# Kernel tuning notes

Hardware: AMD Instinct MI355X
Metric: run time of the kernel (lower is better)

The kernel has to match this reference:

```python
import jax, jax.numpy as jnp
import numpy as np

HEADS = 8
SR = 2
EPS_BN = 1e-5
EPS_LN = 1e-5


def _conv(x, w, b, stride=1, pad=0):
    y = jax.lax.conv_general_dilated(x, w, (stride, stride), [(pad, pad), (pad, pad)],
                                     dimension_numbers=('NCHW', 'OIHW', 'NCHW'))
    return y + b[None, :, None, None]


def _bn(x, g, b):
    # eval-mode BatchNorm with running_mean=0, running_var=1
    return x * (g / jnp.sqrt(1.0 + EPS_BN))[None, :, None, None] + b[None, :, None, None]


def _dwt_haar(x):
    # [B,c,H,W] -> [B,4c,H/2,W/2] stacked as LL,HL,LH,HH (Wave-ViT convention)
    x1 = x[:, :, 0::2, 0::2] / 2
    x2 = x[:, :, 1::2, 0::2] / 2
    x3 = x[:, :, 0::2, 1::2] / 2
    x4 = x[:, :, 1::2, 1::2] / 2
    ll = x1 + x2 + x3 + x4
    hl = -x1 - x2 + x3 + x4
    lh = -x1 + x2 - x3 + x4
    hh = x1 - x2 - x3 + x4
    return jnp.concatenate([ll, hl, lh, hh], axis=1)


def _idwt_haar(y):
    # [B,4c,h,w] -> [B,c,2h,2w], exact inverse of _dwt_haar
    c = y.shape[1] // 4
    ll, hl, lh, hh = y[:, :c], y[:, c:2 * c], y[:, 2 * c:3 * c], y[:, 3 * c:]
    p1 = (ll - hl - lh + hh) / 2  # (0::2, 0::2)
    p2 = (ll - hl + lh - hh) / 2  # (1::2, 0::2)
    p3 = (ll + hl - lh - hh) / 2  # (0::2, 1::2)
    p4 = (ll + hl + lh + hh) / 2  # (1::2, 1::2)
    B, _, h2, w2 = ll.shape
    row0 = jnp.stack([p1, p3], axis=-1)  # even rows
    row1 = jnp.stack([p2, p4], axis=-1)  # odd rows
    out = jnp.stack([row0, row1], axis=3)  # [B,c,h2,2,w2,2]
    return out.reshape(B, c, 2 * h2, 2 * w2)


def setup_inputs() -> dict:
    key = jax.random.key(0)
    ks = jax.random.split(key, 12)
    B, H, W, C = 8, 56, 56, 512
    N = H * W
    c4 = C // 4

    def nrm(k, shp, std):
        return jax.random.normal(k, shp, jnp.float32) * std

    return {
        'x': jax.random.normal(ks[0], (B, N, C), jnp.float32),
        'H': H, 'W': W,
        'reduce_w': nrm(ks[1], (c4, C, 1, 1), (2.0 / c4) ** 0.5),
        'reduce_b': jnp.zeros((c4,), jnp.float32),
        'reduce_g': jnp.ones((c4,), jnp.float32),
        'reduce_beta': jnp.zeros((c4,), jnp.float32),
        'filter_w': nrm(ks[2], (C, C, 3, 3), (2.0 / (9 * C)) ** 0.5),
        'filter_b': jnp.zeros((C,), jnp.float32),
        'filter_g': jnp.ones((C,), jnp.float32),
        'filter_beta': jnp.zeros((C,), jnp.float32),
        'q_w': nrm(ks[3], (C, C), 0.02),
        'q_b': jnp.zeros((C,), jnp.float32),
        'ln_g': jnp.ones((C,), jnp.float32),
        'ln_b': jnp.zeros((C,), jnp.float32),
        'kv_w': nrm(ks[4], (2 * C, C), 0.02),
        'kv_b': jnp.zeros((2 * C,), jnp.float32),
        'kve_w': nrm(ks[5], (C, C, SR, SR), (2.0 / (SR * SR * C)) ** 0.5),
        'kve_b': jnp.zeros((C,), jnp.float32),
        'proj_w': nrm(ks[6], (C, C + c4), 0.02),
        'proj_b': jnp.zeros((C,), jnp.float32),
    }


def reference(x, H, W, reduce_w, reduce_b, reduce_g, reduce_beta,
              filter_w, filter_b, filter_g, filter_beta,
              q_w, q_b, ln_g, ln_b, kv_w, kv_b, kve_w, kve_b, proj_w, proj_b):
    B, N, C = x.shape
    hd = C // HEADS
    scale = hd ** -0.5

    q = (x @ q_w.T + q_b).reshape(B, N, HEADS, hd).transpose(0, 2, 1, 3)  # [B,h,N,d]

    xi = x.reshape(B, H, W, C).transpose(0, 3, 1, 2)  # NCHW
    r = jax.nn.relu(_bn(_conv(xi, reduce_w, reduce_b), reduce_g, reduce_beta))  # [B,C/4,H,W]
    r16 = r.astype(jnp.float16)
    x_dwt = _dwt_haar(r16).astype(jnp.float32)  # [B,C,H/2,W/2]
    x_dwt = jax.nn.relu(_bn(_conv(x_dwt, filter_w, filter_b, pad=1), filter_g, filter_beta))
    x_dwt16 = x_dwt.astype(jnp.float16)
    x_idwt = _idwt_haar(x_dwt16)  # [B,C/4,H,W] fp16
    x_idwt = x_idwt.reshape(B, C // 4, H * W).transpose(0, 2, 1)  # [B,N,C/4]

    x_dwt = x_dwt16.astype(jnp.float32)
    kv_in = _conv(x_dwt, kve_w, kve_b, stride=SR).reshape(B, C, -1).transpose(0, 2, 1)  # [B,M,C]
    mu = kv_in.mean(-1, keepdims=True)
    var = ((kv_in - mu) ** 2).mean(-1, keepdims=True)
    kv_n = (kv_in - mu) / jnp.sqrt(var + EPS_LN) * ln_g + ln_b
    kv = (kv_n @ kv_w.T + kv_b).reshape(B, -1, 2, HEADS, hd).transpose(2, 0, 3, 1, 4)
    k, v = kv[0], kv[1]  # [B,h,M,d]

    attn = jax.nn.softmax(jnp.einsum('bhnd,bhmd->bhnm', q, k) * scale, axis=-1)
    o = jnp.einsum('bhnm,bhmd->bhnd', attn, v).transpose(0, 2, 1, 3).reshape(B, N, C)
    o = jnp.concatenate([o, x_idwt.astype(jnp.float32)], axis=-1)  # [B,N,C+C/4]
    return o @ proj_w.T + proj_b
```

## Files before the change

### kernel.cpp

```cpp
#include <hip/hip_runtime.h>
#include <math.h>


typedef _Float16 half8 __attribute__((ext_vector_type(8)));
typedef float f32x4 __attribute__((ext_vector_type(4)));

static const size_t OFF_X16  = 0;
static const size_t OFF_Q16  = 12845056;
static const size_t OFF_CAT  = 25690112;
static const size_t OFF_R16  = 41746432;
static const size_t OFF_PAD  = 44957696;
static const size_t OFF_DWTB = 48644096;
static const size_t OFF_QRW  = 51855360;
static const size_t OFF_LN16 = 55066624;
static const size_t OFF_KV16 = 55869440;
static const size_t OFF_WT   = 57475072;
static const size_t OFF_KT   = 59834368;
static const size_t OFF_KVW  = 61145088;
static const size_t OFF_PW   = 61669376;
static const size_t OFF_VT   = 62062592;
static const size_t OFF_PART = 62980096;

#define BN_RSQ 0.9999950000374997f
#define SCL2   0.1803368801111204f
#define PART_STRIDE 3211264
#define KVE_STRIDE  802816

__device__ __forceinline__ void async_copy16(const _Float16* g, _Float16* l) {
    __builtin_amdgcn_global_load_lds(
        (const __attribute__((address_space(1))) void*)g,
        (__attribute__((address_space(3))) void*)l, 16, 0, 0);
}

#define WAIT4_BARRIER() asm volatile("s_waitcnt vmcnt(4)\n\ts_barrier" ::: "memory")
#define WAIT6_BARRIER() asm volatile("s_waitcnt vmcnt(6)\n\ts_barrier" ::: "memory")
#define WAIT0_BARRIER() asm volatile("s_waitcnt vmcnt(0)\n\ts_barrier" ::: "memory")

template <int ALOAD, int EPI>
__global__ __launch_bounds__(256) void gemm16(
    const _Float16* __restrict__ A, const _Float16* __restrict__ W,
    void* __restrict__ outp, int M, int K, int lda, int ldc,
    const float* __restrict__ bias, void* __restrict__ outp2)
{
    __shared__ _Float16 sA[3][128 * 32];
    __shared__ _Float16 sB[3][128 * 32];
    const int t = threadIdx.x;
    const int lane = t & 63, wid = t >> 6;

    int bx = blockIdx.x, by = blockIdx.y;
    const int m0 = bx * 128, n0 = by * 128;
    const int kbase = blockIdx.z * K;

    const int sr = wid * 16 + (lane >> 2);
    const int sc = (lane & 3) * 8;
    const int stA0 = wid * 512;
    const int stA1 = 2048 + wid * 512;

    const _Float16 *aP0, *aP1;
    if constexpr (ALOAD == 0) {
        int r0 = m0 + sr;      if (r0 > M - 1) r0 = M - 1;
        int r1 = m0 + 64 + sr; if (r1 > M - 1) r1 = M - 1;
        aP0 = A + (size_t)r0 * lda + sc;
        aP1 = A + (size_t)r1 * lda + sc;
    } else {
        int m_ = m0 + sr; if (m_ > M - 1) m_ = M - 1;
        int b_ = m_ / 196, rem = m_ - b_ * 196, i_ = rem / 14, j_ = rem - i_ * 14;
        aP0 = A + ((size_t)(b_ * 784 + 2 * i_ * 28 + 2 * j_)) * 512 + sc;
        m_ = m0 + 64 + sr; if (m_ > M - 1) m_ = M - 1;
        b_ = m_ / 196; rem = m_ - b_ * 196; i_ = rem / 14; j_ = rem - i_ * 14;
        aP1 = A + ((size_t)(b_ * 784 + 2 * i_ * 28 + 2 * j_)) * 512 + sc;
    }
    const int ldw = (ALOAD == 2) ? lda : K;
    const _Float16* bP0 = W + (size_t)(n0 + sr) * ldw + sc;
    const _Float16* bP1 = W + (size_t)(n0 + 64 + sr) * ldw + sc;

    const int mw = wid & 1, nw = wid >> 1;
    const int pAoff = (mw * 64 + (lane & 15)) * 32 + (lane >> 4) * 8;
    const int pBoff = (nw * 64 + (lane & 15)) * 32 + (lane >> 4) * 8;

    f32x4 acc[4][4];
#pragma unroll
    for (int i = 0; i < 4; ++i)
#pragma unroll
        for (int j = 0; j < 4; ++j) acc[i][j] = (f32x4)(0.0f);

    auto aoff_of = [&](int k) -> int {
        if constexpr (ALOAD == 0) {
            return k;
        } else {
            int sub = k >> 9; int ky = sub >> 1, kx = sub & 1;
            return (ky * 28 + kx) * 512 + (k & 511);
        }
    };
    auto stage = [&](int ti, int buf) {
        int k = kbase + ti * 32;
        int aOff = aoff_of(k);
        async_copy16(aP0 + aOff, &sA[buf][stA0]);
        async_copy16(aP1 + aOff, &sA[buf][stA1]);
        async_copy16(bP0 + k, &sB[buf][stA0]);
        async_copy16(bP1 + k, &sB[buf][stA1]);
    };

    const int nt = K >> 5;
    stage(0, 0);
    if (nt > 1) { stage(1, 1); WAIT4_BARRIER(); }
    else        { WAIT0_BARRIER(); }

    int cur = 0;
    for (int i = 0; i < nt; ++i) {
        const _Float16* pA = &sA[cur][0] + pAoff;
        const _Float16* pB = &sB[cur][0] + pBoff;
        half8 aF[4], bF[4];
#pragma unroll
        for (int u = 0; u < 4; ++u) aF[u] = *(const half8*)(pA + u * 512);
#pragma unroll
        for (int u = 0; u < 4; ++u) bF[u] = *(const half8*)(pB + u * 512);

        const bool st = (i + 2 < nt);
        if (st) {
            int nb = cur + 2; if (nb >= 3) nb -= 3;
            stage(i + 2, nb);
        }
#pragma unroll
        for (int u = 0; u < 4; ++u)
#pragma unroll
            for (int j = 0; j < 4; ++j)
                acc[u][j] = __builtin_amdgcn_mfma_f32_16x16x32_f16(
                    aF[u], bF[j], acc[u][j], 0, 0, 0);

        if (i + 1 < nt) {
            if (st) WAIT4_BARRIER();
            else    WAIT0_BARRIER();
        }
        ++cur; if (cur == 3) cur = 0;
    }

    const int orow = m0 + mw * 64 + (lane >> 4) * 4;
    const int ocol = n0 + nw * 64 + (lane & 15);
#pragma unroll
    for (int j = 0; j < 4; ++j) {
        int col = ocol + j * 16;
        float bv = 0.0f;
        if constexpr (EPI == 5) bv = bias[col];
#pragma unroll
        for (int i = 0; i < 4; ++i) {
#pragma unroll
            for (int r = 0; r < 4; ++r) {
                int row = orow + i * 16 + r;
                if (row >= M) continue;
                float v = acc[i][j][r] + bv;
                if constexpr (EPI == 3) {
                    ((float*)outp)[(size_t)blockIdx.z * KVE_STRIDE
                                   + (size_t)row * ldc + col] = v;
                } else {
                    if (n0 >= 512) {
                        int hd_ = col - 512;
                        int h_ = hd_ >> 6, d_ = hd_ & 63;
                        int b_ = row / 196, m_ = row - b_ * 196;
                        ((_Float16*)outp2)[((size_t)((b_ * 8 + h_) * 64 + d_)) * 224
                                           + m_] = (_Float16)v;
                    } else {
                        ((_Float16*)outp)[(size_t)row * ldc + col] = (_Float16)v;
                    }
                }
            }
        }
    }
}

template <int EPI>
__global__ __launch_bounds__(256) void gemm16f(
    const _Float16* __restrict__ A, const _Float16* __restrict__ W,
    void* __restrict__ outp, int M, int K, int lda, int ldc,
    const float* __restrict__ bias, const float* __restrict__ bng,
    const float* __restrict__ bnb, const float* __restrict__ bias2,
    void* __restrict__ outp2)
{
    __shared__ _Float16 sA[3][256 * 32];
    __shared__ _Float16 sB[3][128 * 32];
    const int t = threadIdx.x;
    const int lane = t & 63, wid = t >> 6;

    int bx = blockIdx.x, by = blockIdx.y;
    {
        int nwg = gridDim.x * gridDim.y;
        if ((nwg & 7) == 0) {
            int orig = by * gridDim.x + bx;
            int cs = nwg >> 3;
            int wg = (orig & 7) * cs + (orig >> 3);
            by = wg % gridDim.y;
            bx = wg / gridDim.y;
        }
    }
    const int m0 = bx * 256, n0 = by * 128;

    const int sr = wid * 16 + (lane >> 2);
    const int sc = (lane & 3) * 8;
    const int stO = wid * 512;

    const _Float16* aP[4];
#pragma unroll
    for (int g = 0; g < 4; ++g) {
        int r_ = m0 + g * 64 + sr; if (r_ > M - 1) r_ = M - 1;
        aP[g] = A + (size_t)r_ * lda + sc;
    }
    const _Float16* bP0 = W + (size_t)(n0 + sr) * K + sc;
    const _Float16* bP1 = W + (size_t)(n0 + 64 + sr) * K + sc;

    const int mw = wid & 1, nw = wid >> 1;
    const int pAoff = (mw * 128 + (lane & 15)) * 32 + (lane >> 4) * 8;
    const int pBoff = (nw * 64 + (lane & 15)) * 32 + (lane >> 4) * 8;

    f32x4 acc[8][4];
#pragma unroll
    for (int i = 0; i < 8; ++i)
#pragma unroll
        for (int j = 0; j < 4; ++j) acc[i][j] = (f32x4)(0.0f);

    auto stage = [&](int ti, int buf) {
        int k = ti * 32;
#pragma unroll
        for (int g = 0; g < 4; ++g)
            async_copy16(aP[g] + k, &sA[buf][g * 2048 + stO]);
        async_copy16(bP0 + k, &sB[buf][stO]);
        async_copy16(bP1 + k, &sB[buf][2048 + stO]);
    };

    const int nt = K >> 5;
    stage(0, 0);
    stage(1, 1);
    WAIT6_BARRIER();

    int cur = 0;
    for (int i = 0; i < nt; ++i) {
        const _Float16* pA = &sA[cur][0] + pAoff;
        const _Float16* pB = &sB[cur][0] + pBoff;
        half8 aF[8], bF[4];
#pragma unroll
        for (int u = 0; u < 8; ++u) aF[u] = *(const half8*)(pA + u * 512);
#pragma unroll
        for (int u = 0; u < 4; ++u) bF[u] = *(const half8*)(pB + u * 512);

        const bool st = (i + 2 < nt);
        if (st) {
            int nb = cur + 2; if (nb >= 3) nb -= 3;
            stage(i + 2, nb);
        }
#pragma unroll
        for (int u = 0; u < 8; ++u)
#pragma unroll
            for (int j = 0; j < 4; ++j)
                acc[u][j] = __builtin_amdgcn_mfma_f32_16x16x32_f16(
                    aF[u], bF[j], acc[u][j], 0, 0, 0);

        if (i + 1 < nt) {
            if (st) WAIT6_BARRIER();
            else    WAIT0_BARRIER();
        }
        ++cur; if (cur == 3) cur = 0;
    }

    const int orow = m0 + mw * 128 + (lane >> 4) * 4;
    const int ocol = n0 + nw * 64 + (lane & 15);
#pragma unroll
    for (int j = 0; j < 4; ++j) {
        int col = ocol + j * 16;
        float bv = 0.0f, g = 0.0f, b2 = 0.0f;
        if constexpr (EPI == 4) {
            if (n0 >= 512) {
                bv = bias2[col - 512];
                g = bng[col - 512] * BN_RSQ;
                b2 = bnb[col - 512];
            } else {
                bv = bias[col];
            }
        } else {
            bv = bias[col];
        }
#pragma unroll
        for (int i = 0; i < 8; ++i) {
#pragma unroll
            for (int r = 0; r < 4; ++r) {
                int row = orow + i * 16 + r;
                if (row >= M) continue;
                float v = acc[i][j][r] + bv;
                if constexpr (EPI == 0) {
                    __builtin_nontemporal_store(
                        v, (float*)outp + (size_t)row * ldc + col);
                } else {
                    if (n0 >= 512) {
                        v = fmaxf(v * g + b2, 0.0f);
                        ((_Float16*)outp2)[(size_t)row * 128 + (col - 512)] =
                            (_Float16)v;
                    } else {
                        ((_Float16*)outp)[(size_t)row * ldc + col] = (_Float16)v;
                    }
                }
            }
        }
    }
}

__global__ __launch_bounds__(256) void conv_splitk_fat(
    const _Float16* __restrict__ A, const _Float16* __restrict__ W,
    float* __restrict__ partA, float* __restrict__ partB)
{
    __shared__ _Float16 sA[3][256 * 32];
    __shared__ _Float16 sB[3][128 * 32];
    const int t = threadIdx.x;
    const int lane = t & 63, wid = t >> 6;

    int orig = blockIdx.x;
    int wg = (orig & 7) * 50 + (orig >> 3);
    int bx = wg % 25;  int c = wg / 25;
    int by = c & 3,    bz = c >> 2;

    const int m0 = bx * 256, n0 = by * 128;
    const int kbase = bz * 1152;

    const int sr = wid * 16 + (lane >> 2);
    const int sc = (lane & 3) * 8;
    const int stO = wid * 512;

    const _Float16* aP[4];
#pragma unroll
    for (int g = 0; g < 4; ++g) {
        int m_ = m0 + g * 64 + sr; if (m_ > 6271) m_ = 6271;
        int b_ = m_ / 784, rem = m_ - b_ * 784, y_ = rem / 28, x_ = rem - y_ * 28;
        aP[g] = A + ((size_t)(b_ * 900 + (y_ + 1) * 30 + (x_ + 1))) * 512 + sc;
    }
    const _Float16* bP0 = W + (size_t)(n0 + sr) * 4608 + sc;
    const _Float16* bP1 = W + (size_t)(n0 + 64 + sr) * 4608 + sc;

    const int mw = wid & 1, nw = wid >> 1;
    const int pAoff = (mw * 128 + (lane & 15)) * 32 + (lane >> 4) * 8;
    const int pBoff = (nw * 64 + (lane & 15)) * 32 + (lane >> 4) * 8;

    f32x4 acc[8][4];
#pragma unroll
    for (int i = 0; i < 8; ++i)
#pragma unroll
        for (int j = 0; j < 4; ++j) acc[i][j] = (f32x4)(0.0f);

    auto aoff_of = [&](int k) -> int {
        int sub = k >> 9; int s3 = sub / 3;
        int dy = s3 - 1, dx = sub - s3 * 3 - 1;
        return (dy * 30 + dx) * 512 + (k & 511);
    };
    auto stage = [&](int ti, int buf) {
        int k = kbase + ti * 32;
        int aOff = aoff_of(k);
#pragma unroll
        for (int g = 0; g < 4; ++g)
            async_copy16(aP[g] + aOff, &sA[buf][g * 2048 + stO]);
        async_copy16(bP0 + k, &sB[buf][stO]);
        async_copy16(bP1 + k, &sB[buf][2048 + stO]);
    };

    const int nt = 36;
    stage(0, 0);
    stage(1, 1);
    WAIT6_BARRIER();

    int cur = 0;
    for (int i = 0; i < nt; ++i) {
        const _Float16* pA = &sA[cur][0] + pAoff;
        const _Float16* pB = &sB[cur][0] + pBoff;
        half8 aF[8], bF[4];
#pragma unroll
        for (int u = 0; u < 8; ++u) aF[u] = *(const half8*)(pA + u * 512);
#pragma unroll
        for (int u = 0; u < 4; ++u) bF[u] = *(const half8*)(pB + u * 512);

        const bool st = (i + 2 < nt);
        if (st) {
            int nb = cur + 2; if (nb >= 3) nb -= 3;
            stage(i + 2, nb);
        }
#pragma unroll
        for (int u = 0; u < 8; ++u)
#pragma unroll
            for (int j = 0; j < 4; ++j)
                acc[u][j] = __builtin_amdgcn_mfma_f32_16x16x32_f16(
                    aF[u], bF[j], acc[u][j], 0, 0, 0);

        if (i + 1 < nt) {
            if (st) WAIT6_BARRIER();
            else    WAIT0_BARRIER();
        }
        ++cur; if (cur == 3) cur = 0;
    }

    float* dst = (bz < 2) ? (partA + (size_t)bz * PART_STRIDE)
                          : (partB + (size_t)(bz - 2) * PART_STRIDE);
    const int orow = m0 + mw * 128 + (lane >> 4) * 4;
    const int ocol = n0 + nw * 64 + (lane & 15);
#pragma unroll
    for (int j = 0; j < 4; ++j) {
#pragma unroll
        for (int i = 0; i < 8; ++i) {
#pragma unroll
            for (int r = 0; r < 4; ++r) {
                int row = orow + i * 16 + r;
                if (row < 6272)
                    dst[(size_t)row * 512 + ocol + j * 16] = acc[i][j][r];
            }
        }
    }
}

__global__ __launch_bounds__(128) void conv_epi_idwt(
    const float* __restrict__ pA, const float* __restrict__ pB,
    _Float16* __restrict__ dwtb, _Float16* __restrict__ cat,
    const float* __restrict__ bias, const float* __restrict__ bng,
    const float* __restrict__ bnb)
{
    int p = blockIdx.x;
    int b = p / 784; int rem = p - b * 784;
    int i = rem / 28;  int j = rem - i * 28;
    int c = threadIdx.x;
    size_t base = (size_t)p * 512;
    _Float16 g16[4];
#pragma unroll
    for (int g = 0; g < 4; ++g) {
        int ch = g * 128 + c;
        float s = (pA[base + ch] + pA[PART_STRIDE + base + ch])
                + (pB[base + ch] + pB[PART_STRIDE + base + ch]);
        float v = (s + bias[ch]) * (bng[ch] * BN_RSQ) + bnb[ch];
        g16[g] = (_Float16)fmaxf(v, 0.0f);
        dwtb[base + ch] = g16[g];
    }
    _Float16 ll = g16[0], hl = g16[1], lh = g16[2], hh = g16[3];
    _Float16 h = (_Float16)0.5f;
    _Float16 p1 = (((ll - hl) - lh) + hh) * h;
    _Float16 p2 = (((ll - hl) + lh) - hh) * h;
    _Float16 p3 = (((ll + hl) - lh) - hh) * h;
    _Float16 p4 = (((ll + hl) + lh) + hh) * h;
    int y = 2 * i, x = 2 * j;
    size_t rb = (size_t)b * 3136;
    __builtin_nontemporal_store(p1, &cat[(rb + (size_t)y * 56 + x) * 640 + 512 + c]);
    __builtin_nontemporal_store(p3, &cat[(rb + (size_t)y * 56 + x + 1) * 640 + 512 + c]);
    __builtin_nontemporal_store(p2, &cat[(rb + (size_t)(y + 1) * 56 + x) * 640 + 512 + c]);
    __builtin_nontemporal_store(p4, &cat[(rb + (size_t)(y + 1) * 56 + x + 1) * 640 + 512 + c]);
}

__device__ __forceinline__ void cvt8_at(
    const float* __restrict__ s, _Float16* __restrict__ d, int i)
{
    const float4* sp = (const float4*)(s + (size_t)i * 8);
    float4 a = sp[0], b = sp[1];
    half8 h;
    h[0] = (_Float16)a.x; h[1] = (_Float16)a.y; h[2] = (_Float16)a.z; h[3] = (_Float16)a.w;
    h[4] = (_Float16)b.x; h[5] = (_Float16)b.y; h[6] = (_Float16)b.z; h[7] = (_Float16)b.w;
    *(half8*)(d + (size_t)i * 8) = h;
}

__global__ __launch_bounds__(256) void prep_kernel(
    const float* __restrict__ qw, const float* __restrict__ rw,
    const float* __restrict__ kvw, const float* __restrict__ pw,
    const float* __restrict__ fw, const float* __restrict__ kw,
    const float* __restrict__ x,
    _Float16* __restrict__ qrw16, _Float16* __restrict__ kvw16,
    _Float16* __restrict__ pw16, _Float16* __restrict__ wT,
    _Float16* __restrict__ kT, _Float16* __restrict__ pad,
    _Float16* __restrict__ vt, _Float16* __restrict__ x16)
{
    int bid = blockIdx.x, tid = threadIdx.x;
    if (bid < 128) {
        cvt8_at(qw, qrw16, bid * 256 + tid);
    } else if (bid < 160) {
        cvt8_at(rw, qrw16 + 262144, (bid - 128) * 256 + tid);
    } else if (bid < 416) {
        cvt8_at(kvw, kvw16, (bid - 160) * 256 + tid);
    } else if (bid < 576) {
        cvt8_at(pw, pw16, (bid - 416) * 256 + tid);
    } else if (bid < 9792) {
        int idx = (bid - 576) * 256 + tid;
        int n = idx / 4608; int r = idx - n * 4608;
        int sub = r >> 9; int ci = r & 511;
        wT[idx] = (_Float16)fw[(size_t)n * 4608 + ci * 9 + sub];
    } else if (bid < 13888) {
        int idx = (bid - 9792) * 256 + tid;
        int n = idx >> 11; int r = idx & 2047;
        int sub = r >> 9; int ci = r & 511;
        kT[idx] = (_Float16)kw[((size_t)n << 11) + (ci << 2) + sub];
    } else if (bid < 15688) {
        int i = (bid - 13888) * 256 + tid;
        *(float4*)(pad + (size_t)i * 8) = make_float4(0.f, 0.f, 0.f, 0.f);
    } else if (bid < 16136) {
        int i = (bid - 15688) * 256 + tid;
        *(float4*)(vt + (size_t)i * 8) = make_float4(0.f, 0.f, 0.f, 0.f);
    } else {
        cvt8_at(x, x16, (bid - 16136) * 256 + tid);
    }
}

__global__ __launch_bounds__(128) void dwt_kernel(
    const _Float16* __restrict__ r, _Float16* __restrict__ pad)
{
    int bid = blockIdx.x;
    int b = bid / 784; int rem = bid - b * 784;
    int i = rem / 28;  int j = rem - i * 28;
    int c = threadIdx.x;
    int y = 2 * i, x = 2 * j;
    size_t base = (size_t)b * 3136;
    _Float16 f1 = r[(base + (size_t)y * 56 + x) * 128 + c];
    _Float16 f2 = r[(base + (size_t)(y + 1) * 56 + x) * 128 + c];
    _Float16 f3 = r[(base + (size_t)y * 56 + (x + 1)) * 128 + c];
    _Float16 f4 = r[(base + (size_t)(y + 1) * 56 + (x + 1)) * 128 + c];
    _Float16 h = (_Float16)0.5f;
    _Float16 x1 = f1 * h, x2 = f2 * h, x3 = f3 * h, x4 = f4 * h;
    _Float16 ll = ((x1 + x2) + x3) + x4;
    _Float16 hl = (((-x1) - x2) + x3) + x4;
    _Float16 lh = (((-x1) + x2) - x3) + x4;
    _Float16 hh = ((x1 - x2) - x3) + x4;
    size_t ob = ((size_t)b * 900 + (size_t)(i + 1) * 30 + (j + 1)) * 512;
    pad[ob + c]       = ll;
    pad[ob + 128 + c] = hl;
    pad[ob + 256 + c] = lh;
    pad[ob + 384 + c] = hh;
}

__global__ __launch_bounds__(256) void ln_kernel(
    const float* __restrict__ part, _Float16* __restrict__ o,
    const float* __restrict__ g, const float* __restrict__ bta,
    const float* __restrict__ kvb)
{
    int wave = threadIdx.x >> 6;
    int lane = threadIdx.x & 63;
    int row = blockIdx.x * 4 + wave;
    int c = lane * 8;
    const float* rp = part + (size_t)row * 512 + c;
    float v[8];
#pragma unroll
    for (int i = 0; i < 8; i += 4) {
        float4 a0 = *(const float4*)(rp + i);
        float4 a1 = *(const float4*)(rp + KVE_STRIDE + i);
        float4 a2 = *(const float4*)(rp + 2 * KVE_STRIDE + i);
        float4 a3 = *(const float4*)(rp + 3 * KVE_STRIDE + i);
        v[i + 0] = (a0.x + a1.x) + (a2.x + a3.x) + kvb[c + i + 0];
        v[i + 1] = (a0.y + a1.y) + (a2.y + a3.y) + kvb[c + i + 1];
        v[i + 2] = (a0.z + a1.z) + (a2.z + a3.z) + kvb[c + i + 2];
        v[i + 3] = (a0.w + a1.w) + (a2.w + a3.w) + kvb[c + i + 3];
    }
    float s = ((v[0] + v[1]) + (v[2] + v[3])) + ((v[4] + v[5]) + (v[6] + v[7]));
#pragma unroll
    for (int off = 32; off; off >>= 1) s += __shfl_xor(s, off);
    float mu = s * (1.0f / 512.0f);
    float sq = 0.0f;
#pragma unroll
    for (int i = 0; i < 8; ++i) { v[i] -= mu; sq += v[i] * v[i]; }
#pragma unroll
    for (int off = 32; off; off >>= 1) sq += __shfl_xor(sq, off);
    float inv = 1.0f / sqrtf(sq * (1.0f / 512.0f) + 1e-5f);
    half8 hv;
#pragma unroll
    for (int i = 0; i < 8; ++i) hv[i] = (_Float16)(v[i] * inv * g[c + i] + bta[c + i]);
    *(half8*)(o + (size_t)row * 512 + c) = hv;
}

__global__ __launch_bounds__(256) void attn_mfma(
    const _Float16* __restrict__ q, const _Float16* __restrict__ kv,
    const _Float16* __restrict__ vt, _Float16* __restrict__ cat)
{
    __shared__ _Float16 sK[64][72];
    __shared__ _Float16 sVT[64][72];
    __shared__ _Float16 sP[4][16][40];
    int bid = blockIdx.x;
    int qt = bid % 49;
    int h  = (bid / 49) & 7;
    int b  = bid / 392;
    int n0 = qt * 64;
    int t = threadIdx.x, lane = t & 63, wid = t >> 6;
    int quad = lane >> 4, l16 = lane & 15;

    const _Float16* qp = q + ((size_t)(b * 3136 + n0 + wid * 16 + l16)) * 512
                           + h * 64 + quad * 8;
    half8 aQ0 = *(const half8*)qp;
    half8 aQ1 = *(const half8*)(qp + 32);

    f32x4 oacc[4];
#pragma unroll
    for (int i = 0; i < 4; ++i) oacc[i] = (f32x4)(0.0f);
    float lsum[4] = {0.f, 0.f, 0.f, 0.f};

    const _Float16* vtb = vt + ((size_t)((b * 8 + h) * 64)) * 224;

    for (int c0 = 0; c0 < 224; c0 += 64) {
        __syncthreads();
#pragma unroll
        for (int it = 0; it < 2; ++it) {
            int slot = t + 256 * it;
            int row = slot >> 3, c8 = (slot & 7) * 8;
            int m = c0 + row; if (m > 195) m = 195;
            *(half8*)&sK[row][c8] =
                *(const half8*)(kv + ((size_t)(b * 196 + m)) * 1024 + h * 64 + c8);
        }
#pragma unroll
        for (int it = 0; it < 2; ++it) {
            int slot = t + 256 * it;
            int row = slot >> 3, c8 = (slot & 7) * 8;
            *(half8*)&sVT[row][c8] =
                *(const half8*)(vtb + (size_t)row * 224 + c0 + c8);
        }
        __syncthreads();

#pragma unroll
        for (int sc = 0; sc < 64; sc += 32) {
            half8 bk00 = *(const half8*)&sK[sc + l16][quad * 8];
            half8 bk01 = *(const half8*)&sK[sc + l16][32 + quad * 8];
            half8 bk10 = *(const half8*)&sK[sc + 16 + l16][quad * 8];
            half8 bk11 = *(const half8*)&sK[sc + 16 + l16][32 + quad * 8];
            f32x4 s0 = (f32x4)(0.0f), s1 = (f32x4)(0.0f);
            s0 = __builtin_amdgcn_mfma_f32_16x16x32_f16(aQ0, bk00, s0, 0, 0, 0);
            s0 = __builtin_amdgcn_mfma_f32_16x16x32_f16(aQ1, bk01, s0, 0, 0, 0);
            s1 = __builtin_amdgcn_mfma_f32_16x16x32_f16(aQ0, bk10, s1, 0, 0, 0);
            s1 = __builtin_amdgcn_mfma_f32_16x16x32_f16(aQ1, bk11, s1, 0, 0, 0);

            int col0 = c0 + sc + l16;
            float msk0 = (col0 < 196) ? 0.0f : -INFINITY;
            float msk1 = (col0 + 16 < 196) ? 0.0f : -INFINITY;
            float p0[4], p1[4];
#pragma unroll
            for (int r = 0; r < 4; ++r) {
                p0[r] = exp2f(s0[r] * SCL2 + msk0);
                p1[r] = exp2f(s1[r] * SCL2 + msk1);
                lsum[r] += p0[r] + p1[r];
            }
#pragma unroll
            for (int r = 0; r < 4; ++r) {
                sP[wid][quad * 4 + r][l16]      = (_Float16)p0[r];
                sP[wid][quad * 4 + r][16 + l16] = (_Float16)p1[r];
            }
            half8 aP = *(const half8*)&sP[wid][l16][quad * 8];
            half8 bv0 = *(const half8*)&sVT[l16][sc + quad * 8];
            half8 bv1 = *(const half8*)&sVT[16 + l16][sc + quad * 8];
            half8 bv2 = *(const half8*)&sVT[32 + l16][sc + quad * 8];
            half8 bv3 = *(const half8*)&sVT[48 + l16][sc + quad * 8];
            oacc[0] = __builtin_amdgcn_mfma_f32_16x16x32_f16(aP, bv0, oacc[0], 0, 0, 0);
            oacc[1] = __builtin_amdgcn_mfma_f32_16x16x32_f16(aP, bv1, oacc[1], 0, 0, 0);
            oacc[2] = __builtin_amdgcn_mfma_f32_16x16x32_f16(aP, bv2, oacc[2], 0, 0, 0);
            oacc[3] = __builtin_amdgcn_mfma_f32_16x16x32_f16(aP, bv3, oacc[3], 0, 0, 0);
        }
    }

    float inv[4];
#pragma unroll
    for (int r = 0; r < 4; ++r) {
        float s = lsum[r];
        s += __shfl_xor(s, 1);
        s += __shfl_xor(s, 2);
        s += __shfl_xor(s, 4);
        s += __shfl_xor(s, 8);
        inv[r] = 1.0f / s;
    }
#pragma unroll
    for (int r = 0; r < 4; ++r) {
        size_t rowoff = ((size_t)(b * 3136 + n0 + wid * 16 + quad * 4 + r)) * 640
                        + h * 64 + l16;
#pragma unroll
        for (int tv = 0; tv < 4; ++tv)
            cat[rowoff + tv * 16] = (_Float16)(oacc[tv][r] * inv[r]);
    }
}

extern "C" void kernel_launch(void* const* d_in, const int* in_sizes, int n_in,
                              void* d_out, int out_size, void* d_ws, size_t ws_size,
                              hipStream_t stream)
{
    const float* x           = (const float*)d_in[0];
    const float* reduce_w    = (const float*)d_in[3];
    const float* reduce_b    = (const float*)d_in[4];
    const float* reduce_g    = (const float*)d_in[5];
    const float* reduce_beta = (const float*)d_in[6];
    const float* filter_w    = (const float*)d_in[7];
    const float* filter_b    = (const float*)d_in[8];
    const float* filter_g    = (const float*)d_in[9];
    const float* filter_beta = (const float*)d_in[10];
    const float* q_w         = (const float*)d_in[11];
    const float* q_b         = (const float*)d_in[12];
    const float* ln_g        = (const float*)d_in[13];
    const float* ln_b        = (const float*)d_in[14];
    const float* kv_w        = (const float*)d_in[15];
    const float* kv_b        = (const float*)d_in[16];
    const float* kve_w       = (const float*)d_in[17];
    const float* kve_b       = (const float*)d_in[18];
    const float* proj_w      = (const float*)d_in[19];
    const float* proj_b      = (const float*)d_in[20];
    float* out = (float*)d_out;
    _Float16* hws = (_Float16*)d_ws;

    _Float16* x16    = hws + OFF_X16;
    _Float16* q16    = hws + OFF_Q16;
    _Float16* cat16  = hws + OFF_CAT;
    _Float16* r16    = hws + OFF_R16;
    _Float16* pad16  = hws + OFF_PAD;
    _Float16* dwtb16 = hws + OFF_DWTB;
    _Float16* qrw16  = hws + OFF_QRW;
    _Float16* ln16   = hws + OFF_LN16;
    _Float16* kv16   = hws + OFF_KV16;
    _Float16* wT16   = hws + OFF_WT;
    _Float16* kT16   = hws + OFF_KT;
    _Float16* kvw16  = hws + OFF_KVW;
    _Float16* pw16   = hws + OFF_PW;
    _Float16* vt16   = hws + OFF_VT;
    float*    partA  = (float*)(hws + OFF_X16);
    float*    partB  = (float*)(hws + OFF_PART);
    float*    kvepart = (float*)(hws + OFF_X16);

    prep_kernel<<<dim3(22408), dim3(256), 0, stream>>>(
        q_w, reduce_w, kv_w, proj_w, filter_w, kve_w, x,
        qrw16, kvw16, pw16, wT16, kT16, pad16, vt16, x16);

    gemm16f<4><<<dim3(98, 5), dim3(256), 0, stream>>>(
        x16, qrw16, q16, 25088, 512, 512, 512, q_b, reduce_g, reduce_beta,
        reduce_b, r16);

    dwt_kernel<<<dim3(6272), dim3(128), 0, stream>>>(r16, pad16);

    conv_splitk_fat<<<dim3(400), dim3(256), 0, stream>>>(pad16, wT16, partA, partB);

    conv_epi_idwt<<<dim3(6272), dim3(128), 0, stream>>>(
        partA, partB, dwtb16, cat16, filter_b, filter_g, filter_beta);

    gemm16<2, 3><<<dim3(13, 4, 4), dim3(256), 0, stream>>>(
        dwtb16, kT16, kvepart, 1568, 512, 2048, 512, nullptr, nullptr);

    ln_kernel<<<dim3(392), dim3(256), 0, stream>>>(kvepart, ln16, ln_g, ln_b, kve_b);

    gemm16<0, 5><<<dim3(13, 8), dim3(256), 0, stream>>>(
        ln16, kvw16, kv16, 1568, 512, 512, 1024, kv_b, vt16);

    attn_mfma<<<dim3(3136), dim3(256), 0, stream>>>(q16, kv16, vt16, cat16);

    gemm16f<0><<<dim3(98, 4), dim3(256), 0, stream>>>(
        cat16, pw16, out, 25088, 640, 640, 512, proj_b, nullptr, nullptr,
        nullptr, nullptr);
}
```

Before: 443.2 us.

## Shrink GEMM and conv tiles to 128x128 with eight waves, add MFMA priority hints

The fat 256x128 GEMM and split-K conv kernels become 128x128 tiles run by 512 threads (eight waves), each wave computing a 64x32 sub-tile with fewer accumulators. Grids double to raise occupancy and spread work across more CUs, at the cost of less data reuse per tile and more LDS traffic per FLOP. Attention MFMA blocks are also wrapped in s_setprio to favour the matrix instructions during scheduling. The conv kernel drops its row clamp and bounds check, which relies on 6272 rows dividing evenly into 128-row tiles.

```diff
diff --git a/kernel.cpp b/kernel.cpp
--- a/kernel.cpp
+++ b/kernel.cpp
@@ -33,7 +33,7 @@
 }
 
 #define WAIT4_BARRIER() asm volatile("s_waitcnt vmcnt(4)\n\ts_barrier" ::: "memory")
-#define WAIT6_BARRIER() asm volatile("s_waitcnt vmcnt(6)\n\ts_barrier" ::: "memory")
+#define WAIT2_BARRIER() asm volatile("s_waitcnt vmcnt(2)\n\ts_barrier" ::: "memory")
 #define WAIT0_BARRIER() asm volatile("s_waitcnt vmcnt(0)\n\ts_barrier" ::: "memory")
 
 template <int ALOAD, int EPI>
@@ -169,14 +169,14 @@
 }
 
 template <int EPI>
-__global__ __launch_bounds__(256) void gemm16f(
+__global__ __launch_bounds__(512) void gemm16w8(
     const _Float16* __restrict__ A, const _Float16* __restrict__ W,
     void* __restrict__ outp, int M, int K, int lda, int ldc,
     const float* __restrict__ bias, const float* __restrict__ bng,
     const float* __restrict__ bnb, const float* __restrict__ bias2,
     void* __restrict__ outp2)
 {
-    __shared__ _Float16 sA[3][256 * 32];
+    __shared__ _Float16 sA[3][128 * 32];
     __shared__ _Float16 sB[3][128 * 32];
     const int t = threadIdx.x;
     const int lane = t & 63, wid = t >> 6;
@@ -192,54 +192,46 @@
             bx = wg / gridDim.y;
         }
     }
-    const int m0 = bx * 256, n0 = by * 128;
+    const int m0 = bx * 128, n0 = by * 128;
 
     const int sr = wid * 16 + (lane >> 2);
     const int sc = (lane & 3) * 8;
     const int stO = wid * 512;
 
-    const _Float16* aP[4];
-#pragma unroll
-    for (int g = 0; g < 4; ++g) {
-        int r_ = m0 + g * 64 + sr; if (r_ > M - 1) r_ = M - 1;
-        aP[g] = A + (size_t)r_ * lda + sc;
-    }
-    const _Float16* bP0 = W + (size_t)(n0 + sr) * K + sc;
-    const _Float16* bP1 = W + (size_t)(n0 + 64 + sr) * K + sc;
+    int r0 = m0 + sr; if (r0 > M - 1) r0 = M - 1;
+    const _Float16* aP = A + (size_t)r0 * lda + sc;
+    const _Float16* bP = W + (size_t)(n0 + sr) * K + sc;
 
     const int mw = wid & 1, nw = wid >> 1;
-    const int pAoff = (mw * 128 + (lane & 15)) * 32 + (lane >> 4) * 8;
-    const int pBoff = (nw * 64 + (lane & 15)) * 32 + (lane >> 4) * 8;
-
-    f32x4 acc[8][4];
-#pragma unroll
-    for (int i = 0; i < 8; ++i)
-#pragma unroll
-        for (int j = 0; j < 4; ++j) acc[i][j] = (f32x4)(0.0f);
+    const int pAoff = (mw * 64 + (lane & 15)) * 32 + (lane >> 4) * 8;
+    const int pBoff = (nw * 32 + (lane & 15)) * 32 + (lane >> 4) * 8;
+
+    f32x4 acc[4][2];
+#pragma unroll
+    for (int i = 0; i < 4; ++i)
+#pragma unroll
+        for (int j = 0; j < 2; ++j) acc[i][j] = (f32x4)(0.0f);
 
     auto stage = [&](int ti, int buf) {
         int k = ti * 32;
-#pragma unroll
-        for (int g = 0; g < 4; ++g)
-            async_copy16(aP[g] + k, &sA[buf][g * 2048 + stO]);
-        async_copy16(bP0 + k, &sB[buf][stO]);
-        async_copy16(bP1 + k, &sB[buf][2048 + stO]);
+        async_copy16(aP + k, &sA[buf][stO]);
+        async_copy16(bP + k, &sB[buf][stO]);
     };
 
     const int nt = K >> 5;
     stage(0, 0);
     stage(1, 1);
-    WAIT6_BARRIER();
+    WAIT2_BARRIER();
 
     int cur = 0;
     for (int i = 0; i < nt; ++i) {
         const _Float16* pA = &sA[cur][0] + pAoff;
         const _Float16* pB = &sB[cur][0] + pBoff;
-        half8 aF[8], bF[4];
-#pragma unroll
-        for (int u = 0; u < 8; ++u) aF[u] = *(const half8*)(pA + u * 512);
-#pragma unroll
-        for (int u = 0; u < 4; ++u) bF[u] = *(const half8*)(pB + u * 512);
+        half8 aF[4], bF[2];
+#pragma unroll
+        for (int u = 0; u < 4; ++u) aF[u] = *(const half8*)(pA + u * 512);
+#pragma unroll
+        for (int v = 0; v < 2; ++v) bF[v] = *(const half8*)(pB + v * 512);
 
         const bool st = (i + 2 < nt);
         if (st) {
@@ -247,25 +239,25 @@
             stage(i + 2, nb);
         }
 #pragma unroll
-        for (int u = 0; u < 8; ++u)
-#pragma unroll
-            for (int j = 0; j < 4; ++j)
-                acc[u][j] = __builtin_amdgcn_mfma_f32_16x16x32_f16(
-                    aF[u], bF[j], acc[u][j], 0, 0, 0);
+        for (int u = 0; u < 4; ++u)
+#pragma unroll
+            for (int v = 0; v < 2; ++v)
+                acc[u][v] = __builtin_amdgcn_mfma_f32_16x16x32_f16(
+                    aF[u], bF[v], acc[u][v], 0, 0, 0);
 
         if (i + 1 < nt) {
-            if (st) WAIT6_BARRIER();
+            if (st) WAIT2_BARRIER();
             else    WAIT0_BARRIER();
         }
         ++cur; if (cur == 3) cur = 0;
     }
 
-    const int orow = m0 + mw * 128 + (lane >> 4) * 4;
-    const int ocol = n0 + nw * 64 + (lane & 15);
-#pragma unroll
-    for (int j = 0; j < 4; ++j) {
-        int col = ocol + j * 16;
-        float bv = 0.0f, g = 0.0f, b2 = 0.0f;
+    const int orow = m0 + mw * 64 + (lane >> 4) * 4;
+    const int ocol = n0 + nw * 32 + (lane & 15);
+#pragma unroll
+    for (int v = 0; v < 2; ++v) {
+        int col = ocol + v * 16;
+        float bv, g = 0.0f, b2 = 0.0f;
         if constexpr (EPI == 4) {
             if (n0 >= 512) {
                 bv = bias2[col - 512];
@@ -278,22 +270,22 @@
             bv = bias[col];
         }
 #pragma unroll
-        for (int i = 0; i < 8; ++i) {
+        for (int u = 0; u < 4; ++u) {
 #pragma unroll
             for (int r = 0; r < 4; ++r) {
-                int row = orow + i * 16 + r;
+                int row = orow + u * 16 + r;
                 if (row >= M) continue;
-                float v = acc[i][j][r] + bv;
+                float v2 = acc[u][v][r] + bv;
                 if constexpr (EPI == 0) {
                     __builtin_nontemporal_store(
-                        v, (float*)outp + (size_t)row * ldc + col);
+                        v2, (float*)outp + (size_t)row * ldc + col);
                 } else {
                     if (n0 >= 512) {
-                        v = fmaxf(v * g + b2, 0.0f);
+                        v2 = fmaxf(v2 * g + b2, 0.0f);
                         ((_Float16*)outp2)[(size_t)row * 128 + (col - 512)] =
-                            (_Float16)v;
+                            (_Float16)v2;
                     } else {
-                        ((_Float16*)outp)[(size_t)row * ldc + col] = (_Float16)v;
+                        ((_Float16*)outp)[(size_t)row * ldc + col] = (_Float16)v2;
                     }
                 }
             }
@@ -301,46 +293,41 @@
     }
 }
 
-__global__ __launch_bounds__(256) void conv_splitk_fat(
+__global__ __launch_bounds__(512) void conv_splitk(
     const _Float16* __restrict__ A, const _Float16* __restrict__ W,
     float* __restrict__ partA, float* __restrict__ partB)
 {
-    __shared__ _Float16 sA[3][256 * 32];
+    __shared__ _Float16 sA[3][128 * 32];
     __shared__ _Float16 sB[3][128 * 32];
     const int t = threadIdx.x;
     const int lane = t & 63, wid = t >> 6;
 
     int orig = blockIdx.x;
-    int wg = (orig & 7) * 50 + (orig >> 3);
-    int bx = wg % 25;  int c = wg / 25;
+    int wg = (orig & 7) * 98 + (orig >> 3);
+    int bx = wg % 49;  int c = wg / 49;
     int by = c & 3,    bz = c >> 2;
 
-    const int m0 = bx * 256, n0 = by * 128;
+    const int m0 = bx * 128, n0 = by * 128;
     const int kbase = bz * 1152;
 
     const int sr = wid * 16 + (lane >> 2);
     const int sc = (lane & 3) * 8;
     const int stO = wid * 512;
 
-    const _Float16* aP[4];
-#pragma unroll
-    for (int g = 0; g < 4; ++g) {
-        int m_ = m0 + g * 64 + sr; if (m_ > 6271) m_ = 6271;
-        int b_ = m_ / 784, rem = m_ - b_ * 784, y_ = rem / 28, x_ = rem - y_ * 28;
-        aP[g] = A + ((size_t)(b_ * 900 + (y_ + 1) * 30 + (x_ + 1))) * 512 + sc;
-    }
-    const _Float16* bP0 = W + (size_t)(n0 + sr) * 4608 + sc;
-    const _Float16* bP1 = W + (size_t)(n0 + 64 + sr) * 4608 + sc;
+    int m_ = m0 + sr;
+    int b_ = m_ / 784, rem = m_ - b_ * 784, y_ = rem / 28, x_ = rem - y_ * 28;
+    const _Float16* aP = A + ((size_t)(b_ * 900 + (y_ + 1) * 30 + (x_ + 1))) * 512 + sc;
+    const _Float16* bP = W + (size_t)(n0 + sr) * 4608 + sc;
 
     const int mw = wid & 1, nw = wid >> 1;
-    const int pAoff = (mw * 128 + (lane & 15)) * 32 + (lane >> 4) * 8;
-    const int pBoff = (nw * 64 + (lane & 15)) * 32 + (lane >> 4) * 8;
-
-    f32x4 acc[8][4];
-#pragma unroll
-    for (int i = 0; i < 8; ++i)
-#pragma unroll
-        for (int j = 0; j < 4; ++j) acc[i][j] = (f32x4)(0.0f);
+    const int pAoff = (mw * 64 + (lane & 15)) * 32 + (lane >> 4) * 8;
+    const int pBoff = (nw * 32 + (lane & 15)) * 32 + (lane >> 4) * 8;
+
+    f32x4 acc[4][2];
+#pragma unroll
+    for (int i = 0; i < 4; ++i)
+#pragma unroll
+        for (int j = 0; j < 2; ++j) acc[i][j] = (f32x4)(0.0f);
 
     auto aoff_of = [&](int k) -> int {
         int sub = k >> 9; int s3 = sub / 3;
@@ -349,28 +336,24 @@
     };
     auto stage = [&](int ti, int buf) {
         int k = kbase + ti * 32;
-        int aOff = aoff_of(k);
-#pragma unroll
-        for (int g = 0; g < 4; ++g)
-            async_copy16(aP[g] + aOff, &sA[buf][g * 2048 + stO]);
-        async_copy16(bP0 + k, &sB[buf][stO]);
-        async_copy16(bP1 + k, &sB[buf][2048 + stO]);
+        async_copy16(aP + aoff_of(k), &sA[buf][stO]);
+        async_copy16(bP + k, &sB[buf][stO]);
     };
 
     const int nt = 36;
     stage(0, 0);
     stage(1, 1);
-    WAIT6_BARRIER();
+    WAIT2_BARRIER();
 
     int cur = 0;
     for (int i = 0; i < nt; ++i) {
         const _Float16* pA = &sA[cur][0] + pAoff;
         const _Float16* pB = &sB[cur][0] + pBoff;
-        half8 aF[8], bF[4];
-#pragma unroll
-        for (int u = 0; u < 8; ++u) aF[u] = *(const half8*)(pA + u * 512);
-#pragma unroll
-        for (int u = 0; u < 4; ++u) bF[u] = *(const half8*)(pB + u * 512);
+        half8 aF[4], bF[2];
+#pragma unroll
+        for (int u = 0; u < 4; ++u) aF[u] = *(const half8*)(pA + u * 512);
+#pragma unroll
+        for (int v = 0; v < 2; ++v) bF[v] = *(const half8*)(pB + v * 512);
 
         const bool st = (i + 2 < nt);
         if (st) {
@@ -378,14 +361,14 @@
             stage(i + 2, nb);
         }
 #pragma unroll
-        for (int u = 0; u < 8; ++u)
-#pragma unroll
-            for (int j = 0; j < 4; ++j)
-                acc[u][j] = __builtin_amdgcn_mfma_f32_16x16x32_f16(
-                    aF[u], bF[j], acc[u][j], 0, 0, 0);
+        for (int u = 0; u < 4; ++u)
+#pragma unroll
+            for (int v = 0; v < 2; ++v)
+                acc[u][v] = __builtin_amdgcn_mfma_f32_16x16x32_f16(
+                    aF[u], bF[v], acc[u][v], 0, 0, 0);
 
         if (i + 1 < nt) {
-            if (st) WAIT6_BARRIER();
+            if (st) WAIT2_BARRIER();
             else    WAIT0_BARRIER();
         }
         ++cur; if (cur == 3) cur = 0;
@@ -393,18 +376,15 @@
 
     float* dst = (bz < 2) ? (partA + (size_t)bz * PART_STRIDE)
                           : (partB + (size_t)(bz - 2) * PART_STRIDE);
-    const int orow = m0 + mw * 128 + (lane >> 4) * 4;
-    const int ocol = n0 + nw * 64 + (lane & 15);
-#pragma unroll
-    for (int j = 0; j < 4; ++j) {
-#pragma unroll
-        for (int i = 0; i < 8; ++i) {
-#pragma unroll
-            for (int r = 0; r < 4; ++r) {
-                int row = orow + i * 16 + r;
-                if (row < 6272)
-                    dst[(size_t)row * 512 + ocol + j * 16] = acc[i][j][r];
-            }
+    const int orow = m0 + mw * 64 + (lane >> 4) * 4;
+    const int ocol = n0 + nw * 32 + (lane & 15);
+#pragma unroll
+    for (int v = 0; v < 2; ++v) {
+#pragma unroll
+        for (int u = 0; u < 4; ++u) {
+#pragma unroll
+            for (int r = 0; r < 4; ++r)
+                dst[(size_t)(orow + u * 16 + r) * 512 + ocol + v * 16] = acc[u][v][r];
         }
     }
 }
@@ -612,10 +592,12 @@
             half8 bk10 = *(const half8*)&sK[sc + 16 + l16][quad * 8];
             half8 bk11 = *(const half8*)&sK[sc + 16 + l16][32 + quad * 8];
             f32x4 s0 = (f32x4)(0.0f), s1 = (f32x4)(0.0f);
+            __builtin_amdgcn_s_setprio(1);
             s0 = __builtin_amdgcn_mfma_f32_16x16x32_f16(aQ0, bk00, s0, 0, 0, 0);
             s0 = __builtin_amdgcn_mfma_f32_16x16x32_f16(aQ1, bk01, s0, 0, 0, 0);
             s1 = __builtin_amdgcn_mfma_f32_16x16x32_f16(aQ0, bk10, s1, 0, 0, 0);
             s1 = __builtin_amdgcn_mfma_f32_16x16x32_f16(aQ1, bk11, s1, 0, 0, 0);
+            __builtin_amdgcn_s_setprio(0);
 
             int col0 = c0 + sc + l16;
             float msk0 = (col0 < 196) ? 0.0f : -INFINITY;
@@ -637,10 +619,12 @@
             half8 bv1 = *(const half8*)&sVT[16 + l16][sc + quad * 8];
             half8 bv2 = *(const half8*)&sVT[32 + l16][sc + quad * 8];
             half8 bv3 = *(const half8*)&sVT[48 + l16][sc + quad * 8];
+            __builtin_amdgcn_s_setprio(1);
             oacc[0] = __builtin_amdgcn_mfma_f32_16x16x32_f16(aP, bv0, oacc[0], 0, 0, 0);
             oacc[1] = __builtin_amdgcn_mfma_f32_16x16x32_f16(aP, bv1, oacc[1], 0, 0, 0);
             oacc[2] = __builtin_amdgcn_mfma_f32_16x16x32_f16(aP, bv2, oacc[2], 0, 0, 0);
             oacc[3] = __builtin_amdgcn_mfma_f32_16x16x32_f16(aP, bv3, oacc[3], 0, 0, 0);
+            __builtin_amdgcn_s_setprio(0);
         }
     }
 
@@ -712,13 +696,13 @@
         q_w, reduce_w, kv_w, proj_w, filter_w, kve_w, x,
         qrw16, kvw16, pw16, wT16, kT16, pad16, vt16, x16);
 
-    gemm16f<4><<<dim3(98, 5), dim3(256), 0, stream>>>(
+    gemm16w8<4><<<dim3(196, 5), dim3(512), 0, stream>>>(
         x16, qrw16, q16, 25088, 512, 512, 512, q_b, reduce_g, reduce_beta,
         reduce_b, r16);
 
     dwt_kernel<<<dim3(6272), dim3(128), 0, stream>>>(r16, pad16);
 
-    conv_splitk_fat<<<dim3(400), dim3(256), 0, stream>>>(pad16, wT16, partA, partB);
+    conv_splitk<<<dim3(784), dim3(512), 0, stream>>>(pad16, wT16, partA, partB);
 
     conv_epi_idwt<<<dim3(6272), dim3(128), 0, stream>>>(
         partA, partB, dwtb16, cat16, filter_b, filter_g, filter_beta);
@@ -733,7 +717,7 @@
 
     attn_mfma<<<dim3(3136), dim3(256), 0, stream>>>(q16, kv16, vt16, cat16);
 
-    gemm16f<0><<<dim3(98, 4), dim3(256), 0, stream>>>(
+    gemm16w8<0><<<dim3(196, 4), dim3(512), 0, stream>>>(
         cat16, pw16, out, 25088, 640, 640, 512, proj_b, nullptr, nullptr,
         nullptr, nullptr);
 }
```

New measurement: 380.9 us. -14.1%, faster.
